# Performance work log

Hardware: AMD Instinct MI355X
Metric: run time of the kernel (lower is better)

## Reference

```python
import jax, jax.numpy as jnp
import numpy as np

N_NODES = 100000
N_EDGES = 1600000
IN_DIM, HID_DIM, OUT_DIM = 128, 256, 128


def gcn_conv(x, src, dst, W, b, n):
    # PyG GCNConv: linear transform, add self-loops, symmetric normalization,
    # scatter-sum aggregation over destination nodes, then bias.
    h = x @ W  # [n, d_out]
    loops = jnp.arange(n, dtype=src.dtype)
    s = jnp.concatenate([src, loops])
    d = jnp.concatenate([dst, loops])
    deg = jax.ops.segment_sum(jnp.ones_like(d, dtype=h.dtype), d, num_segments=n)
    dinv = jnp.where(deg > 0, jax.lax.rsqrt(deg), 0.0)
    norm = dinv[s] * dinv[d]  # [E+n]
    msg = h[s] * norm[:, None]  # gather + scale
    out = jax.ops.segment_sum(msg, d, num_segments=n)  # scatter-reduce
    return out + b


def layer_norm(x, gamma, beta, eps=1e-5):
    mu = jnp.mean(x, axis=-1, keepdims=True)
    var = jnp.mean(jnp.square(x - mu), axis=-1, keepdims=True)
    return (x - mu) * jax.lax.rsqrt(var + eps) * gamma + beta


def setup_inputs() -> dict:
    key = jax.random.key(0)
    ks = jax.random.split(key, 8)
    x = jax.random.normal(ks[0], (N_NODES, IN_DIM), dtype=jnp.float32)
    edge_index = jax.random.randint(ks[1], (2, N_EDGES), 0, N_NODES, dtype=jnp.int64)
    W1 = jax.random.normal(ks[2], (IN_DIM, HID_DIM), dtype=jnp.float32) * (1.0 / np.sqrt(IN_DIM))
    b1 = jnp.zeros((HID_DIM,), dtype=jnp.float32)
    W2 = jax.random.normal(ks[3], (HID_DIM, OUT_DIM), dtype=jnp.float32) * (1.0 / np.sqrt(HID_DIM))
    b2 = jnp.zeros((OUT_DIM,), dtype=jnp.float32)
    gamma = jnp.ones((OUT_DIM,), dtype=jnp.float32)
    beta = jnp.zeros((OUT_DIM,), dtype=jnp.float32)
    return {"x": x, "edge_index": edge_index, "W1": W1, "b1": b1,
            "W2": W2, "b2": b2, "gamma": gamma, "beta": beta}


def reference(x, edge_index, W1, b1, W2, b2, gamma, beta):
    n = x.shape[0]
    src, dst = edge_index[0], edge_index[1]
    h = gcn_conv(x, src, dst, W1, b1, n)
    h = jax.nn.relu(h)
    # dropout(p=0.1) is identity in eval mode
    h = gcn_conv(h, src, dst, W2, b2, n)
    return layer_norm(h, gamma, beta)
```

## Files before the change

### kernel.cpp

```cpp
#include <hip/hip_runtime.h>
#include <hip/hip_fp16.h>
#include <stdint.h>

#define N_NODES 100000
#define N_EDGES 1600000
#define IN_DIM  128
#define HID_DIM 256
#define OUT_DIM 128
#define RS 264
#define NBUCK 391
#define EPB   4096
#define PADB  5120
#define PB    391
#define WB    256

typedef __attribute__((ext_vector_type(8))) _Float16 f16x8;
typedef __attribute__((ext_vector_type(4))) float f32x4;

__device__ __forceinline__ int clampi(int v) {
    v = v < 0 ? 0 : v;
    return v >= N_NODES ? N_NODES - 1 : v;
}
__device__ __forceinline__ float2 h2f2(uint32_t u) {
    union { uint32_t u; __half2 h; } c; c.u = u;
    return __half22float2(c.h);
}
__device__ __forceinline__ uint32_t packh(float a, float b) {
    union { __half2 h; uint32_t u; } c; c.h = __floats2half2_rn(a, b);
    return c.u;
}
__device__ __forceinline__ uint16_t f2h(float a) {
    union { __half h; uint16_t s; } c; c.h = __float2half_rn(a);
    return c.s;
}

__device__ __forceinline__ int src_at(const int* ei, int isI64, int e) {
    return clampi(isI64 ? ei[2 * (size_t)e] : ei[e]);
}
__device__ __forceinline__ int dst_at(const int* ei, int isI64, int e) {
    return clampi(isI64 ? ei[2 * (size_t)N_EDGES + 2 * (size_t)e]
                        : ei[(size_t)N_EDGES + e]);
}


__global__ __launch_bounds__(256) void partition_kernel(const int* __restrict__ ei,
                                                        int* __restrict__ cursor,
                                                        uint32_t* __restrict__ recs,
                                                        const float* __restrict__ W1,
                                                        uint16_t* __restrict__ W1t,
                                                        const float* __restrict__ W2,
                                                        uint16_t* __restrict__ W2t) {
    if (blockIdx.x >= PB) {
        int idx = (blockIdx.x - PB) * 256 + threadIdx.x;
        if (idx < IN_DIM * HID_DIM) {
            int k = idx / HID_DIM, n = idx - k * HID_DIM;
            W1t[n * IN_DIM + k] = f2h(W1[idx]);
        } else {
            int j = idx - IN_DIM * HID_DIM;
            int k = j / OUT_DIM, n = j - k * OUT_DIM;
            W2t[n * HID_DIM + k] = f2h(W2[j]);
        }
        return;
    }
    __shared__ int hist[NBUCK];
    __shared__ int gBase[NBUCK];
    __shared__ int s_flag;
    int tid = threadIdx.x;
    if (tid == 0) {
        int z = 1;
        #pragma unroll
        for (int i = 0; i < 16; ++i)
            if (ei[2 * i + 1] != 0) z = 0;
        s_flag = z;
    }
    for (int b = tid; b < NBUCK; b += 256) hist[b] = 0;
    __syncthreads();
    int isI64 = s_flag;
    int base = blockIdx.x * EPB;
    int srcs[16], dsts[16], slots[16];
    #pragma unroll
    for (int r = 0; r < 16; ++r) {
        int e = base + r * 256 + tid;
        slots[r] = -1;
        srcs[r] = 0; dsts[r] = 0;
        if (e < N_EDGES) {
            srcs[r] = src_at(ei, isI64, e);
            dsts[r] = dst_at(ei, isI64, e);
            slots[r] = atomicAdd(&hist[dsts[r] >> 8], 1);
        }
    }
    __syncthreads();
    for (int b = tid; b < NBUCK; b += 256)
        if (hist[b] > 0) gBase[b] = atomicAdd(&cursor[b], hist[b]);
    __syncthreads();
    #pragma unroll
    for (int r = 0; r < 16; ++r) {
        if (slots[r] >= 0) {
            int b = dsts[r] >> 8;
            int pos = gBase[b] + slots[r];
            if (pos < PADB)
                recs[(size_t)b * PADB + pos] =
                    ((uint32_t)srcs[r] << 8) | (uint32_t)(dsts[r] & 255);
        }
    }
}


__global__ __launch_bounds__(256) void build_kernel(const uint32_t* __restrict__ recs,
                                                    const int* __restrict__ cursor,
                                                    int* __restrict__ row_ptr,
                                                    float* __restrict__ dinv,
                                                    int* __restrict__ colv,
                                                    const float* __restrict__ x,
                                                    uint2* __restrict__ xsout) {
    __shared__ uint32_t lrec[PADB];
    __shared__ int cnt[256];
    __shared__ int lofs[256];
    __shared__ int cur[256];
    __shared__ int scanT[256];
    int b = blockIdx.x, tid = threadIdx.x;
    int nb = cursor[b]; if (nb > PADB) nb = PADB;
    int pv = 0;
    for (int j = tid; j < b; j += 256) {
        int c = cursor[j];
        pv += (c > PADB) ? PADB : c;
    }
    cnt[tid] = 0; cur[tid] = 0;
    scanT[tid] = pv;
    __syncthreads();
    for (int off = 128; off > 0; off >>= 1) {
        if (tid < off) scanT[tid] += scanT[tid + off];
        __syncthreads();
    }
    int cbase = scanT[0];
    __syncthreads();
    for (int i = tid; i < nb; i += 256) {
        uint32_t r = recs[(size_t)b * PADB + i];
        lrec[i] = r;
        atomicAdd(&cnt[r & 255], 1);
    }
    __syncthreads();
    scanT[tid] = cnt[tid];
    __syncthreads();
    for (int off = 1; off < 256; off <<= 1) {
        int x2 = (tid >= off) ? scanT[tid - off] : 0;
        __syncthreads();
        if (tid >= off) scanT[tid] += x2;
        __syncthreads();
    }
    lofs[tid] = tid ? scanT[tid - 1] : 0;
    int node = b * 256 + tid;
    if (node < N_NODES) {
        row_ptr[node] = cbase + lofs[tid];
        dinv[node] = rsqrtf((float)(cnt[tid] + 1));
    }
    if (b == NBUCK - 1 && tid == 0) row_ptr[N_NODES] = cbase + nb;
    __syncthreads();
    for (int i = tid; i < nb; i += 256) {
        uint32_t r = lrec[i];
        int id = (int)(r & 255);
        int slot = atomicAdd(&cur[id], 1);
        colv[cbase + lofs[id] + slot] = (int)(r >> 8);
    }
    const float4* x4 = (const float4*)x + (size_t)b * 8192;
    uint2* xo = xsout + (size_t)b * 8192;
    int lim = (N_NODES - b * 256) * 32; if (lim > 8192) lim = 8192;
    for (int j = tid; j < lim; j += 256) {
        float d = rsqrtf((float)(cnt[j >> 5] + 1));
        float4 v = x4[j];
        uint2 o;
        o.x = packh(d * v.x, d * v.y);
        o.y = packh(d * v.z, d * v.w);
        xo[j] = o;
    }
}


template<bool LN>
__global__ __launch_bounds__(256) void agg_kernel(const uint4* __restrict__ rows,
                                                  const int* __restrict__ row_ptr,
                                                  const int* __restrict__ colv,
                                                  const float* __restrict__ dinv,
                                                  const float* __restrict__ bias,
                                                  const float* __restrict__ gamma,
                                                  const float* __restrict__ beta,
                                                  float* __restrict__ out,
                                                  uint4* __restrict__ out16) {
    int node = blockIdx.x * 16 + (threadIdx.x >> 4);
    if (node >= N_NODES) return;
    int l = threadIdx.x & 15;
    const char* base = (const char*)rows + ((unsigned)l << 4);
    float di = dinv[node];
    float acc[8];
    {
        uint4 u = *(const uint4*)(base + ((unsigned)node << 8));
        float2 f0 = h2f2(u.x), f1 = h2f2(u.y), f2 = h2f2(u.z), f3 = h2f2(u.w);
        acc[0] = f0.x; acc[1] = f0.y; acc[2] = f1.x; acc[3] = f1.y;
        acc[4] = f2.x; acc[5] = f2.y; acc[6] = f3.x; acc[7] = f3.y;
    }
    int e = row_ptr[node], e1 = row_ptr[node + 1];
    int s0 = 0, s1 = 0, s2 = 0, s3 = 0;
    if (e     < e1) s0 = colv[e];
    if (e + 1 < e1) s1 = colv[e + 1];
    if (e + 2 < e1) s2 = colv[e + 2];
    if (e + 3 < e1) s3 = colv[e + 3];
    while (e + 4 <= e1) {
        uint4 v0 = *(const uint4*)(base + ((unsigned)s0 << 8));
        uint4 v1 = *(const uint4*)(base + ((unsigned)s1 << 8));
        uint4 v2 = *(const uint4*)(base + ((unsigned)s2 << 8));
        uint4 v3 = *(const uint4*)(base + ((unsigned)s3 << 8));
        int p0 = (e + 4 < e1) ? e + 4 : e;
        int p1 = (e + 5 < e1) ? e + 5 : e;
        int p2 = (e + 6 < e1) ? e + 6 : e;
        int p3 = (e + 7 < e1) ? e + 7 : e;
        int t0 = colv[p0], t1 = colv[p1], t2 = colv[p2], t3 = colv[p3];
        {
            float2 f0 = h2f2(v0.x), f1 = h2f2(v0.y), f2 = h2f2(v0.z), f3 = h2f2(v0.w);
            acc[0] += f0.x; acc[1] += f0.y; acc[2] += f1.x; acc[3] += f1.y;
            acc[4] += f2.x; acc[5] += f2.y; acc[6] += f3.x; acc[7] += f3.y;
        }
        {
            float2 f0 = h2f2(v1.x), f1 = h2f2(v1.y), f2 = h2f2(v1.z), f3 = h2f2(v1.w);
            acc[0] += f0.x; acc[1] += f0.y; acc[2] += f1.x; acc[3] += f1.y;
            acc[4] += f2.x; acc[5] += f2.y; acc[6] += f3.x; acc[7] += f3.y;
        }
        {
            float2 f0 = h2f2(v2.x), f1 = h2f2(v2.y), f2 = h2f2(v2.z), f3 = h2f2(v2.w);
            acc[0] += f0.x; acc[1] += f0.y; acc[2] += f1.x; acc[3] += f1.y;
            acc[4] += f2.x; acc[5] += f2.y; acc[6] += f3.x; acc[7] += f3.y;
        }
        {
            float2 f0 = h2f2(v3.x), f1 = h2f2(v3.y), f2 = h2f2(v3.z), f3 = h2f2(v3.w);
            acc[0] += f0.x; acc[1] += f0.y; acc[2] += f1.x; acc[3] += f1.y;
            acc[4] += f2.x; acc[5] += f2.y; acc[6] += f3.x; acc[7] += f3.y;
        }
        s0 = t0; s1 = t1; s2 = t2; s3 = t3; e += 4;
    }
    int r = e1 - e;
    if (r > 0) {
        uint4 v = *(const uint4*)(base + ((unsigned)s0 << 8));
        float2 f0 = h2f2(v.x), f1 = h2f2(v.y), f2 = h2f2(v.z), f3 = h2f2(v.w);
        acc[0] += f0.x; acc[1] += f0.y; acc[2] += f1.x; acc[3] += f1.y;
        acc[4] += f2.x; acc[5] += f2.y; acc[6] += f3.x; acc[7] += f3.y;
    }
    if (r > 1) {
        uint4 v = *(const uint4*)(base + ((unsigned)s1 << 8));
        float2 f0 = h2f2(v.x), f1 = h2f2(v.y), f2 = h2f2(v.z), f3 = h2f2(v.w);
        acc[0] += f0.x; acc[1] += f0.y; acc[2] += f1.x; acc[3] += f1.y;
        acc[4] += f2.x; acc[5] += f2.y; acc[6] += f3.x; acc[7] += f3.y;
    }
    if (r > 2) {
        uint4 v = *(const uint4*)(base + ((unsigned)s2 << 8));
        float2 f0 = h2f2(v.x), f1 = h2f2(v.y), f2 = h2f2(v.z), f3 = h2f2(v.w);
        acc[0] += f0.x; acc[1] += f0.y; acc[2] += f1.x; acc[3] += f1.y;
        acc[4] += f2.x; acc[5] += f2.y; acc[6] += f3.x; acc[7] += f3.y;
    }
    if (!LN) {
        uint4 o;
        o.x = packh(acc[0] * di, acc[1] * di);
        o.y = packh(acc[2] * di, acc[3] * di);
        o.z = packh(acc[4] * di, acc[5] * di);
        o.w = packh(acc[6] * di, acc[7] * di);
        out16[(size_t)node * 16 + l] = o;
    } else {
        const float4* b4 = (const float4*)(bias + l * 8);
        float4 bb0 = b4[0], bb1 = b4[1];
        float v[8];
        v[0] = acc[0] * di + bb0.x; v[1] = acc[1] * di + bb0.y;
        v[2] = acc[2] * di + bb0.z; v[3] = acc[3] * di + bb0.w;
        v[4] = acc[4] * di + bb1.x; v[5] = acc[5] * di + bb1.y;
        v[6] = acc[6] * di + bb1.z; v[7] = acc[7] * di + bb1.w;
        float s = 0.f;
        #pragma unroll
        for (int j = 0; j < 8; ++j) s += v[j];
        #pragma unroll
        for (int o = 8; o > 0; o >>= 1) s += __shfl_xor(s, o, 64);
        float mu = s * (1.0f / 128.0f);
        float q = 0.f;
        #pragma unroll
        for (int j = 0; j < 8; ++j) { v[j] -= mu; q += v[j] * v[j]; }
        #pragma unroll
        for (int o = 8; o > 0; o >>= 1) q += __shfl_xor(q, o, 64);
        float rstd = rsqrtf(q * (1.0f / 128.0f) + 1e-5f);
        const float4* g4 = (const float4*)(gamma + l * 8);
        const float4* t4 = (const float4*)(beta + l * 8);
        float4 g0 = g4[0], g1 = g4[1], t0 = t4[0], t1 = t4[1];
        float* orow = out + (size_t)node * 128 + l * 8;
        f32x4 o0, o1;
        o0.x = v[0] * rstd * g0.x + t0.x; o0.y = v[1] * rstd * g0.y + t0.y;
        o0.z = v[2] * rstd * g0.z + t0.z; o0.w = v[3] * rstd * g0.w + t0.w;
        o1.x = v[4] * rstd * g1.x + t1.x; o1.y = v[5] * rstd * g1.y + t1.y;
        o1.z = v[6] * rstd * g1.z + t1.z; o1.w = v[7] * rstd * g1.w + t1.w;
        __builtin_nontemporal_store(o0, (f32x4*)orow);
        __builtin_nontemporal_store(o1, (f32x4*)(orow + 4));
    }
}


__global__ __launch_bounds__(256) void fused_gemm_kernel(const uint16_t* __restrict__ A16,
                                                         const uint16_t* __restrict__ W1t,
                                                         const float* __restrict__ b1,
                                                         const uint16_t* __restrict__ W2t,
                                                         const float* __restrict__ dinv,
                                                         uint16_t* __restrict__ G16, int M) {
    __shared__ __align__(16) uint16_t Hs[64 * RS];
    int lane = threadIdx.x & 63;
    int wave = threadIdx.x >> 6;
    int r15 = lane & 15;
    int quad = lane >> 4;
    int kofs = quad * 8;
    int blk_row = blockIdx.x * 64;

    f16x8 a[4][4];
    #pragma unroll
    for (int mt = 0; mt < 4; ++mt) {
        bool valid = (blk_row + mt * 16) < M;
        int row = valid ? (blk_row + mt * 16 + r15) : 0;
        const uint16_t* arow = A16 + (size_t)row * IN_DIM + kofs;
        #pragma unroll
        for (int ks = 0; ks < 4; ++ks)
            a[mt][ks] = *(const f16x8*)(arow + ks * 32);
    }

    #pragma unroll
    for (int nt = 0; nt < 4; ++nt) {
        int ncol = (wave * 4 + nt) * 16 + r15;
        const uint16_t* bp = W1t + (size_t)ncol * IN_DIM + kofs;
        f32x4 acc[4];
        #pragma unroll
        for (int mt = 0; mt < 4; ++mt) acc[mt] = (f32x4){0.f, 0.f, 0.f, 0.f};
        #pragma unroll
        for (int ks = 0; ks < 4; ++ks) {
            f16x8 bv = *(const f16x8*)(bp + ks * 32);
            #pragma unroll
            for (int mt = 0; mt < 4; ++mt)
                acc[mt] = __builtin_amdgcn_mfma_f32_16x16x32_f16(a[mt][ks], bv, acc[mt], 0, 0, 0);
        }
        float bb = b1[ncol];
        #pragma unroll
        for (int mt = 0; mt < 4; ++mt) {
            #pragma unroll
            for (int r = 0; r < 4; ++r) {
                int lrow = mt * 16 + quad * 4 + r;
                Hs[lrow * RS + ncol] = f2h(fmaxf(acc[mt][r] + bb, 0.f));
            }
        }
    }
    __syncthreads();

    #pragma unroll
    for (int nt = 0; nt < 2; ++nt) {
        int ncol = (wave * 2 + nt) * 16 + r15;
        const uint16_t* bp = W2t + (size_t)ncol * HID_DIM + kofs;
        f16x8 b2[8];
        #pragma unroll
        for (int ks = 0; ks < 8; ++ks)
            b2[ks] = *(const f16x8*)(bp + ks * 32);
        f32x4 acc[4];
        #pragma unroll
        for (int mt = 0; mt < 4; ++mt) acc[mt] = (f32x4){0.f, 0.f, 0.f, 0.f};
        #pragma unroll
        for (int ks = 0; ks < 8; ++ks) {
            #pragma unroll
            for (int mt = 0; mt < 4; ++mt) {
                f16x8 av = *(const f16x8*)(Hs + (mt * 16 + r15) * RS + ks * 32 + kofs);
                acc[mt] = __builtin_amdgcn_mfma_f32_16x16x32_f16(av, b2[ks], acc[mt], 0, 0, 0);
            }
        }
        #pragma unroll
        for (int mt = 0; mt < 4; ++mt) {
            if ((blk_row + mt * 16) < M) {
                #pragma unroll
                for (int r = 0; r < 4; ++r) {
                    int row = blk_row + mt * 16 + quad * 4 + r;
                    G16[(size_t)row * OUT_DIM + ncol] = f2h(dinv[row] * acc[mt][r]);
                }
            }
        }
    }
}


extern "C" void kernel_launch(void* const* d_in, const int* in_sizes, int n_in,
                              void* d_out, int out_size, void* d_ws, size_t ws_size,
                              hipStream_t stream) {
    const float* x     = (const float*)d_in[0];
    const int*   ei    = (const int*)d_in[1];
    const float* W1    = (const float*)d_in[2];
    const float* b1    = (const float*)d_in[3];
    const float* W2    = (const float*)d_in[4];
    const float* b2    = (const float*)d_in[5];
    const float* gamma = (const float*)d_in[6];
    const float* beta  = (const float*)d_in[7];

    char* ws = (char*)d_ws;
    size_t off = 0;
    auto alloc = [&](size_t bytes) -> void* {
        void* p = ws + off;
        off += (bytes + 511) & ~(size_t)511;
        return p;
    };
    int*      cursor  = (int*)alloc((size_t)NBUCK * 4);
    int*      row_ptr = (int*)alloc((size_t)(N_NODES + 1) * 4);
    float*    dinv    = (float*)alloc((size_t)N_NODES * 4);
    uint16_t* W1t     = (uint16_t*)alloc((size_t)IN_DIM * HID_DIM * 2);
    uint16_t* W2t     = (uint16_t*)alloc((size_t)HID_DIM * OUT_DIM * 2);
    int*      colv    = (int*)alloc((size_t)N_EDGES * 4);
    void*     big     = alloc((size_t)N_NODES * IN_DIM * 2);
    uint32_t* recs    = (uint32_t*)big;
    uint16_t* g16     = (uint16_t*)big;
    if (ws_size < off) return;

    uint2*    xs16 = (uint2*)d_out;
    uint16_t* xa16 = (uint16_t*)d_out + (size_t)N_NODES * IN_DIM;

    const int AB = (N_NODES + 15) / 16;
    const int GB = (N_NODES + 63) / 64;

    hipMemsetAsync(cursor, 0, (size_t)NBUCK * 4, stream);
    partition_kernel<<<PB + WB, 256, 0, stream>>>(ei, cursor, recs, W1, W1t, W2, W2t);
    build_kernel<<<NBUCK, 256, 0, stream>>>(recs, cursor, row_ptr, dinv, colv, x, xs16);
    agg_kernel<false><<<AB, 256, 0, stream>>>((const uint4*)xs16, row_ptr, colv, dinv,
                                              nullptr, nullptr, nullptr,
                                              nullptr, (uint4*)xa16);
    fused_gemm_kernel<<<GB, 256, 0, stream>>>(xa16, W1t, b1, W2t, dinv, g16, N_NODES);
    agg_kernel<true><<<AB, 256, 0, stream>>>((const uint4*)g16, row_ptr, colv, dinv,
                                             b2, gamma, beta, (float*)d_out, nullptr);
}
```

Measured before the change: 327.3 us.

## Split x scaling out of build kernel and use wave-shuffle scans

Moves the dinv-scaled fp16 conversion of x out of the 391-block CSR build kernel into a separate, fully parallel elementwise kernel. The build kernel's shared-memory tree reductions and scans are replaced with wavefront shuffle reductions, and the staged records are kept in registers instead of a 20KB LDS buffer. This cuts barriers and LDS use in build and lets the x conversion spread across the whole GPU, at the cost of one extra launch and a dinv read.

```diff
diff --git a/kernel.cpp b/kernel.cpp
--- a/kernel.cpp
+++ b/kernel.cpp
@@ -110,68 +110,79 @@
                                                     const int* __restrict__ cursor,
                                                     int* __restrict__ row_ptr,
                                                     float* __restrict__ dinv,
-                                                    int* __restrict__ colv,
-                                                    const float* __restrict__ x,
-                                                    uint2* __restrict__ xsout) {
-    __shared__ uint32_t lrec[PADB];
+                                                    int* __restrict__ colv) {
     __shared__ int cnt[256];
     __shared__ int lofs[256];
     __shared__ int cur[256];
-    __shared__ int scanT[256];
+    __shared__ int wsum[8];
     int b = blockIdx.x, tid = threadIdx.x;
+    int lane = tid & 63, wv = tid >> 6;
     int nb = cursor[b]; if (nb > PADB) nb = PADB;
     int pv = 0;
     for (int j = tid; j < b; j += 256) {
         int c = cursor[j];
         pv += (c > PADB) ? PADB : c;
     }
+    #pragma unroll
+    for (int o = 32; o > 0; o >>= 1) pv += __shfl_xor(pv, o, 64);
     cnt[tid] = 0; cur[tid] = 0;
-    scanT[tid] = pv;
-    __syncthreads();
-    for (int off = 128; off > 0; off >>= 1) {
-        if (tid < off) scanT[tid] += scanT[tid + off];
-        __syncthreads();
-    }
-    int cbase = scanT[0];
-    __syncthreads();
-    for (int i = tid; i < nb; i += 256) {
-        uint32_t r = recs[(size_t)b * PADB + i];
-        lrec[i] = r;
-        atomicAdd(&cnt[r & 255], 1);
-    }
-    __syncthreads();
-    scanT[tid] = cnt[tid];
-    __syncthreads();
-    for (int off = 1; off < 256; off <<= 1) {
-        int x2 = (tid >= off) ? scanT[tid - off] : 0;
-        __syncthreads();
-        if (tid >= off) scanT[tid] += x2;
-        __syncthreads();
-    }
-    lofs[tid] = tid ? scanT[tid - 1] : 0;
+    if (lane == 0) wsum[wv] = pv;
+    __syncthreads();
+    int cbase = wsum[0] + wsum[1] + wsum[2] + wsum[3];
+    uint32_t rr[20];
+    #pragma unroll
+    for (int r = 0; r < 20; ++r) {
+        int i = r * 256 + tid;
+        rr[r] = 0xFFFFFFFFu;
+        if (i < nb) {
+            rr[r] = recs[(size_t)b * PADB + i];
+            atomicAdd(&cnt[rr[r] & 255], 1);
+        }
+    }
+    __syncthreads();
+    int v = cnt[tid];
+    int inc = v;
+    #pragma unroll
+    for (int o = 1; o < 64; o <<= 1) {
+        int t = __shfl_up(inc, o, 64);
+        if (lane >= o) inc += t;
+    }
+    if (lane == 63) wsum[4 + wv] = inc;
+    __syncthreads();
+    int woff = 0;
+    #pragma unroll
+    for (int w = 0; w < 4; ++w) if (w < wv) woff += wsum[4 + w];
+    int excl = woff + inc - v;
+    lofs[tid] = excl;
     int node = b * 256 + tid;
     if (node < N_NODES) {
-        row_ptr[node] = cbase + lofs[tid];
-        dinv[node] = rsqrtf((float)(cnt[tid] + 1));
+        row_ptr[node] = cbase + excl;
+        dinv[node] = rsqrtf((float)(v + 1));
     }
     if (b == NBUCK - 1 && tid == 0) row_ptr[N_NODES] = cbase + nb;
     __syncthreads();
-    for (int i = tid; i < nb; i += 256) {
-        uint32_t r = lrec[i];
-        int id = (int)(r & 255);
-        int slot = atomicAdd(&cur[id], 1);
-        colv[cbase + lofs[id] + slot] = (int)(r >> 8);
-    }
-    const float4* x4 = (const float4*)x + (size_t)b * 8192;
-    uint2* xo = xsout + (size_t)b * 8192;
-    int lim = (N_NODES - b * 256) * 32; if (lim > 8192) lim = 8192;
-    for (int j = tid; j < lim; j += 256) {
-        float d = rsqrtf((float)(cnt[j >> 5] + 1));
-        float4 v = x4[j];
+    #pragma unroll
+    for (int r = 0; r < 20; ++r) {
+        if (rr[r] != 0xFFFFFFFFu) {
+            int id = (int)(rr[r] & 255);
+            int slot = atomicAdd(&cur[id], 1);
+            colv[cbase + lofs[id] + slot] = (int)(rr[r] >> 8);
+        }
+    }
+}
+
+
+__global__ __launch_bounds__(256) void xscale_kernel(const float* __restrict__ x,
+                                                     const float* __restrict__ dinv,
+                                                     uint2* __restrict__ xs16) {
+    int idx = blockIdx.x * 256 + threadIdx.x;
+    if (idx < N_NODES * 32) {
+        float d = dinv[idx >> 5];
+        float4 v = ((const float4*)x)[idx];
         uint2 o;
         o.x = packh(d * v.x, d * v.y);
         o.y = packh(d * v.z, d * v.w);
-        xo[j] = o;
+        xs16[idx] = o;
     }
 }
 
@@ -416,10 +427,12 @@
 
     const int AB = (N_NODES + 15) / 16;
     const int GB = (N_NODES + 63) / 64;
+    const int XB = (N_NODES * 32 + 255) / 256;
 
     hipMemsetAsync(cursor, 0, (size_t)NBUCK * 4, stream);
     partition_kernel<<<PB + WB, 256, 0, stream>>>(ei, cursor, recs, W1, W1t, W2, W2t);
-    build_kernel<<<NBUCK, 256, 0, stream>>>(recs, cursor, row_ptr, dinv, colv, x, xs16);
+    build_kernel<<<NBUCK, 256, 0, stream>>>(recs, cursor, row_ptr, dinv, colv);
+    xscale_kernel<<<XB, 256, 0, stream>>>(x, dinv, xs16);
     agg_kernel<false><<<AB, 256, 0, stream>>>((const uint4*)xs16, row_ptr, colv, dinv,
                                               nullptr, nullptr, nullptr,
                                               nullptr, (uint4*)xa16);
```

New measurement: 316.7 us. 1.03x faster.
